# Kernel optimization log

Hardware: AMD Instinct MI355X
Metric: run time of the kernel (lower is better)

Reference implementation:

```python
import jax, jax.numpy as jnp
import numpy as np

B, L, D, H = 4, 1024, 1024, 16
DH = D // H
NEG = -1e9
EPS = 1e-5


def setup_inputs() -> dict:
    key = jax.random.key(0)
    ks = jax.random.split(key, 12)
    s = 1.0 / np.sqrt(D)
    inp = {
        "Q": jax.random.normal(ks[0], (B, L, D), jnp.float32),
        "K": jax.random.normal(ks[1], (B, L, D), jnp.float32),
        "V": jax.random.normal(ks[2], (B, L, D), jnp.float32),
        "K_mask": jnp.ones((B, L), jnp.int32),
        "WQ": jax.random.normal(ks[3], (D, D), jnp.float32) * s,
        "bQ": jnp.zeros((D,), jnp.float32),
        "WK": jax.random.normal(ks[4], (D, D), jnp.float32) * s,
        "bK": jnp.zeros((D,), jnp.float32),
        "WV": jax.random.normal(ks[5], (D, D), jnp.float32) * s,
        "bV": jnp.zeros((D,), jnp.float32),
        "WO": jax.random.normal(ks[6], (D, D), jnp.float32) * s,
        "bO": jnp.zeros((D,), jnp.float32),
        "ln_g": jnp.ones((D,), jnp.float32),
        "ln_b": jnp.zeros((D,), jnp.float32),
    }
    return inp


def _mha(Q, K, V, K_mask, WQ, bQ, WK, bK, WV, bV, WO, bO, ln_g, ln_b):
    # projections  [B,L,D]
    q = Q @ WQ + bQ
    k = K @ WK + bK
    v = V @ WV + bV
    # split heads -> [B,H,L,dh]
    q = q.reshape(B, L, H, DH).transpose(0, 2, 1, 3)
    k = k.reshape(B, L, H, DH).transpose(0, 2, 1, 3)
    v = v.reshape(B, L, H, DH).transpose(0, 2, 1, 3)
    # scaled dot product, masked softmax over keys
    scores = jnp.einsum("bhqd,bhkd->bhqk", q, k) / jnp.sqrt(jnp.float32(DH))
    mask = (K_mask > 0)[:, None, None, :]  # [B,1,1,Lk]
    scores = jnp.where(mask, scores, NEG)
    attn = jax.nn.softmax(scores, axis=-1)  # dropout is identity at inference
    ctx = jnp.einsum("bhqk,bhkd->bhqd", attn, v)
    ctx = ctx.transpose(0, 2, 1, 3).reshape(B, L, D)
    # output layer: dense + residual + layernorm
    out = ctx @ WO + bO
    x = out + Q
    mu = jnp.mean(x, axis=-1, keepdims=True)
    var = jnp.var(x, axis=-1, keepdims=True)
    return (x - mu) * jax.lax.rsqrt(var + EPS) * ln_g + ln_b


def reference(Q, K, V, K_mask, WQ, bQ, WK, bK, WV, bV, WO, bO, ln_g, ln_b):
    return _mha(Q, K, V, K_mask, WQ, bQ, WK, bK, WV, bV, WO, bO, ln_g, ln_b)
```

## Files before the change

### kernel.cpp

```cpp
#include <hip/hip_runtime.h>
#include <hip/hip_bf16.h>
#include <stdint.h>

#define Bn 4
#define Ln 1024
#define Dn 1024
#define Hn 16
#define DHn 64
#define Mn (Bn*Ln)

typedef __attribute__((ext_vector_type(8))) short short8v;
typedef __attribute__((ext_vector_type(4))) float floatx4;

__device__ __forceinline__ unsigned short f2b(float f){
  union { float f; unsigned u; } v; v.f = f;
  unsigned r = (v.u + 0x7FFFu + ((v.u >> 16) & 1u)) >> 16;
  return (unsigned short)r;
}
__device__ __forceinline__ unsigned short f2b_fast(float f){
  __hip_bfloat16 h = __float2bfloat16(f);
  return *reinterpret_cast<unsigned short*>(&h);
}

typedef const unsigned __attribute__((address_space(1)))* gas1_t;
typedef unsigned __attribute__((address_space(3)))* las3_t;
__device__ __forceinline__ void gload16(const void* g, void* l){
  __builtin_amdgcn_global_load_lds((gas1_t)(uintptr_t)g, (las3_t)(uintptr_t)l, 16, 0, 0);
}

__global__ __launch_bounds__(256) void tobf16x3_k(const float* __restrict__ x0,
    const float* __restrict__ x1, const float* __restrict__ x2,
    unsigned short* __restrict__ o0, unsigned short* __restrict__ o1,
    unsigned short* __restrict__ o2)
{
  const int i = blockIdx.x * 256 + threadIdx.x;
  const int sel = i >> 20, idx = i & 0xFFFFF;
  const float* x = sel == 0 ? x0 : (sel == 1 ? x1 : x2);
  unsigned short* o = sel == 0 ? o0 : (sel == 1 ? o1 : o2);
  float4 v = reinterpret_cast<const float4*>(x)[idx];
  union { unsigned short u[4]; uint2 q; } p;
  p.u[0] = f2b(v.x); p.u[1] = f2b(v.y); p.u[2] = f2b(v.z); p.u[3] = f2b(v.w);
  reinterpret_cast<uint2*>(o)[idx] = p.q;
}

__global__ __launch_bounds__(256) void wconv4_k(const float* __restrict__ W0,
    const float* __restrict__ W1, const float* __restrict__ W2,
    const float* __restrict__ W3, unsigned short* __restrict__ Wt0,
    unsigned short* __restrict__ Wt1, unsigned short* __restrict__ Wt2,
    unsigned short* __restrict__ Wt3)
{
  const float* W; unsigned short* Wt;
  switch (blockIdx.z){
    case 0: W = W0; Wt = Wt0; break;
    case 1: W = W1; Wt = Wt1; break;
    case 2: W = W2; Wt = Wt2; break;
    default: W = W3; Wt = Wt3; break;
  }
  __shared__ float tile[64][65];
  const int nb = blockIdx.x * 64, kb = blockIdx.y * 64;
  const int tx = threadIdx.x & 63, ty = threadIdx.x >> 6;
  #pragma unroll
  for (int r = 0; r < 64; r += 4)
    tile[r + ty][tx] = W[(size_t)(kb + r + ty) * 1024 + nb + tx];
  __syncthreads();
  #pragma unroll
  for (int r = 0; r < 64; r += 4)
    Wt[(size_t)(nb + r + ty) * 1024 + kb + tx] = f2b(tile[tx][r + ty]);
}

template<int MODE>
__device__ __forceinline__ void gemm8_core(const unsigned short* __restrict__ Ab,
    const unsigned short* __restrict__ Btp, const float* __restrict__ bias,
    void* __restrict__ outp, float scale, unsigned short* lds, int nt, int mt)
{
  const int tid = threadIdx.x;
  const int lane = tid & 63, wave = tid >> 6;
  const int wr = wave >> 2, wc = wave & 3;
  const int lg = lane >> 4, lr = lane & 15;
  const int m0 = mt * 256, n0 = nt * 256;

  const unsigned short* gAb[2];
  const unsigned short* gBb[2];
  int ldso[2];
  #pragma unroll
  for (int i = 0; i < 2; i++){
    int c = tid + 512 * i;
    int g16 = c >> 6, lrr = c & 15, lgg = (c >> 4) & 3;
    int row = g16 * 16 + lrr;
    gAb[i] = Ab  + (size_t)(m0 + row) * 1024 + lgg * 8;
    gBb[i] = Btp + (size_t)(n0 + row) * 1024 + lgg * 8;
    ldso[i] = c * 8;
  }
  auto stageA = [&](int sg){
    unsigned short* slot = lds + (sg & 3) * 16384;
    const int kcol = (sg >> 1) * 64 + (sg & 1) * 32;
    #pragma unroll
    for (int i = 0; i < 2; i++) gload16(gAb[i] + kcol, &slot[ldso[i]]);
  };
  auto stageB = [&](int sg){
    unsigned short* slot = lds + (sg & 3) * 16384 + 8192;
    const int kcol = (sg >> 1) * 64 + (sg & 1) * 32;
    #pragma unroll
    for (int i = 0; i < 2; i++) gload16(gBb[i] + kcol, &slot[ldso[i]]);
  };

  floatx4 acc[8][4] = {};

  stageA(0); stageB(0); stageA(1); stageB(1); stageA(2); stageB(2);

  for (int t = 0; t < 16; t++){
    unsigned short* slot0 = lds + ((2 * t) & 3) * 16384;
    unsigned short* slot1 = lds + ((2 * t + 1) & 3) * 16384;
    short8v af[4], bf[4];
    if (t < 15) asm volatile("s_waitcnt vmcnt(4)" ::: "memory");
    else        asm volatile("s_waitcnt vmcnt(0)" ::: "memory");
    __builtin_amdgcn_s_barrier();
    __builtin_amdgcn_sched_barrier(0);
    if (t < 15) stageA(2 * t + 3);
    #pragma unroll
    for (int n = 0; n < 4; n++)
      bf[n] = *reinterpret_cast<const short8v*>(&slot0[8192 + ((wc * 4 + n) * 64 + lane) * 8]);
    #pragma unroll
    for (int i2 = 0; i2 < 4; i2++)
      af[i2] = *reinterpret_cast<const short8v*>(&slot0[((wr * 8 + i2) * 64 + lane) * 8]);
    __builtin_amdgcn_s_setprio(1);
    #pragma unroll
    for (int a = 0; a < 4; a++)
      #pragma unroll
      for (int n = 0; n < 4; n++)
        acc[a][n] = __builtin_amdgcn_mfma_f32_16x16x32_bf16(af[a], bf[n], acc[a][n], 0, 0, 0);
    __builtin_amdgcn_s_setprio(0);
    if (t < 15) stageB(2 * t + 3);
    #pragma unroll
    for (int i2 = 0; i2 < 4; i2++)
      af[i2] = *reinterpret_cast<const short8v*>(&slot0[((wr * 8 + 4 + i2) * 64 + lane) * 8]);
    __builtin_amdgcn_s_setprio(1);
    #pragma unroll
    for (int a = 0; a < 4; a++)
      #pragma unroll
      for (int n = 0; n < 4; n++)
        acc[4 + a][n] = __builtin_amdgcn_mfma_f32_16x16x32_bf16(af[a], bf[n], acc[4 + a][n], 0, 0, 0);
    __builtin_amdgcn_s_setprio(0);
    __builtin_amdgcn_sched_barrier(0);
    __builtin_amdgcn_s_barrier();
    __builtin_amdgcn_sched_barrier(0);
    if (t < 14) stageA(2 * t + 4);
    #pragma unroll
    for (int n = 0; n < 4; n++)
      bf[n] = *reinterpret_cast<const short8v*>(&slot1[8192 + ((wc * 4 + n) * 64 + lane) * 8]);
    #pragma unroll
    for (int i2 = 0; i2 < 4; i2++)
      af[i2] = *reinterpret_cast<const short8v*>(&slot1[((wr * 8 + i2) * 64 + lane) * 8]);
    __builtin_amdgcn_s_setprio(1);
    #pragma unroll
    for (int a = 0; a < 4; a++)
      #pragma unroll
      for (int n = 0; n < 4; n++)
        acc[a][n] = __builtin_amdgcn_mfma_f32_16x16x32_bf16(af[a], bf[n], acc[a][n], 0, 0, 0);
    __builtin_amdgcn_s_setprio(0);
    if (t < 14) stageB(2 * t + 4);
    #pragma unroll
    for (int i2 = 0; i2 < 4; i2++)
      af[i2] = *reinterpret_cast<const short8v*>(&slot1[((wr * 8 + 4 + i2) * 64 + lane) * 8]);
    __builtin_amdgcn_s_setprio(1);
    #pragma unroll
    for (int a = 0; a < 4; a++)
      #pragma unroll
      for (int n = 0; n < 4; n++)
        acc[4 + a][n] = __builtin_amdgcn_mfma_f32_16x16x32_bf16(af[a], bf[n], acc[4 + a][n], 0, 0, 0);
    __builtin_amdgcn_s_setprio(0);
    __builtin_amdgcn_sched_barrier(0);
  }

  if constexpr (MODE == 2){
    __syncthreads();
    #pragma unroll
    for (int n = 0; n < 4; n++){
      const int gn_l = wc * 64 + n * 16 + lr;
      const float bb = bias[n0 + gn_l];
      const int X = (gn_l & 7) << 3;
      #pragma unroll
      for (int a = 0; a < 8; a++){
        const int gm_l = wr * 128 + a * 16 + lg * 4;
        union { unsigned short u[4]; uint2 q; } pk;
        #pragma unroll
        for (int r = 0; r < 4; r++) pk.u[r] = f2b((acc[a][n][r] + bb) * scale);
        *reinterpret_cast<uint2*>(&lds[gn_l * 256 + (gm_l ^ X)]) = pk.q;
      }
    }
    __syncthreads();
    const int bb2 = m0 >> 10, l0 = m0 & 1023;
    const int row = tid >> 1, colb = (tid & 1) * 128;
    const int h2 = (n0 + row) >> 6, d = (n0 + row) & 63;
    unsigned short* obase = (unsigned short*)outp +
        (((size_t)(bb2 * Hn + h2)) * DHn + d) * Ln + l0 + colb;
    const int XR = (row & 7) << 3;
    #pragma unroll
    for (int g = 0; g < 16; g++){
      short8v v = *reinterpret_cast<const short8v*>(&lds[row * 256 + ((colb + g * 8) ^ XR)]);
      *reinterpret_cast<short8v*>(obase + g * 8) = v;
    }
  } else {
    unsigned short* o = (unsigned short*)outp;
    #pragma unroll
    for (int n = 0; n < 4; n++){
      const int gn = n0 + wc * 64 + n * 16 + lr;
      const float bbv = bias[gn];
      const int h2 = gn >> 6, d = gn & 63;
      #pragma unroll
      for (int a = 0; a < 8; a++){
        const int gm0v = m0 + wr * 128 + a * 16 + lg * 4;
        #pragma unroll
        for (int r = 0; r < 4; r++){
          const int gm = gm0v + r;
          const int bb2 = gm >> 10, l = gm & 1023;
          o[(((size_t)(bb2 * Hn + h2)) * Ln + l) * DHn + d] = f2b((acc[a][n][r] + bbv) * scale);
        }
      }
    }
  }
}

__global__ __launch_bounds__(512, 2) void gemmqkv8_k(
    const unsigned short* __restrict__ A0, const unsigned short* __restrict__ A1,
    const unsigned short* __restrict__ A2, const unsigned short* __restrict__ W0,
    const unsigned short* __restrict__ W1, const unsigned short* __restrict__ W2,
    const float* __restrict__ b0, const float* __restrict__ b1,
    const float* __restrict__ b2, unsigned short* __restrict__ o0,
    unsigned short* __restrict__ o1, unsigned short* __restrict__ o2, float qscl)
{
  __shared__ __align__(16) unsigned short lds[65536];
  const int g = blockIdx.x >> 3;
  const int nt = g & 3;
  const int panel = (g >> 2) * 8 + (blockIdx.x & 7);
  const int z = panel >> 4, mt = panel & 15;
  if (z == 0)
    gemm8_core<0>(A0, W0, b0, o0, qscl, lds, nt, mt);
  else if (z == 1)
    gemm8_core<0>(A1, W1, b1, o1, 1.f, lds, nt, mt);
  else
    gemm8_core<2>(A2, W2, b2, o2, 1.f, lds, nt, mt);
}

__device__ __forceinline__ void gemm_core3(const unsigned short* __restrict__ Ab,
    const unsigned short* __restrict__ Btp, const float* __restrict__ bias,
    float* __restrict__ outp, const float* __restrict__ resid,
    unsigned short* lds, int nt, int mt)
{
  const int tid = threadIdx.x;
  const int lane = tid & 63, wave = tid >> 6;
  const int wr = wave >> 1, wc = wave & 1;
  const int lg = lane >> 4, lr = lane & 15;
  const int m0 = mt * 128, n0 = nt * 128;

  const unsigned short* gA[4];
  const unsigned short* gB[4];
  #pragma unroll
  for (int i = 0; i < 4; i++){
    int c = (wave * 4 + i) * 64 + lane;
    int ks = c >> 9, r16 = (c >> 6) & 7, lhi = (c >> 4) & 3, lrr = c & 15;
    int row = r16 * 16 + lrr, col = ks * 32 + lhi * 8;
    gA[i] = Ab  + (size_t)(m0 + row) * 1024 + col;
    gB[i] = Btp + (size_t)(n0 + row) * 1024 + col;
  }

  floatx4 acc[4][4] = {};

  auto issue = [&](int t){
    unsigned short* bufA = lds + (t % 3) * 16384;
    unsigned short* bufB = bufA + 8192;
    #pragma unroll
    for (int i = 0; i < 4; i++){
      gload16(gA[i] + t * 64, &bufA[(wave * 4 + i) * 512]);
      gload16(gB[i] + t * 64, &bufB[(wave * 4 + i) * 512]);
    }
  };

  issue(0); issue(1);

  for (int kb = 0; kb < 16; kb++){
    unsigned short* bufA = lds + (kb % 3) * 16384;
    unsigned short* bufB = bufA + 8192;
    if (kb < 14){
      issue(kb + 2);
      asm volatile("s_waitcnt vmcnt(16)" ::: "memory");
    } else if (kb == 14){
      asm volatile("s_waitcnt vmcnt(8)" ::: "memory");
    } else {
      asm volatile("s_waitcnt vmcnt(0)" ::: "memory");
    }
    __builtin_amdgcn_s_barrier();
    __builtin_amdgcn_sched_barrier(0);
    #pragma unroll
    for (int ks = 0; ks < 2; ks++){
      short8v af[4], bfr[4];
      #pragma unroll
      for (int m = 0; m < 4; m++)
        af[m] = *reinterpret_cast<const short8v*>(&bufA[((ks * 8 + wr * 4 + m) * 64 + lane) * 8]);
      #pragma unroll
      for (int n = 0; n < 4; n++)
        bfr[n] = *reinterpret_cast<const short8v*>(&bufB[((ks * 8 + wc * 4 + n) * 64 + lane) * 8]);
      #pragma unroll
      for (int m = 0; m < 4; m++)
        #pragma unroll
        for (int n = 0; n < 4; n++)
          acc[m][n] = __builtin_amdgcn_mfma_f32_16x16x32_bf16(af[m], bfr[n], acc[m][n], 0, 0, 0);
    }
    __builtin_amdgcn_sched_barrier(0);
    __builtin_amdgcn_s_barrier();
  }

  #pragma unroll
  for (int n = 0; n < 4; n++){
    const int gn = n0 + wc * 64 + n * 16 + lr;
    const float bb = bias[gn];
    #pragma unroll
    for (int m = 0; m < 4; m++){
      const int gm0 = m0 + wr * 64 + m * 16 + lg * 4;
      #pragma unroll
      for (int r = 0; r < 4; r++){
        const int gm = gm0 + r;
        float v = acc[m][n][r] + bb;
        outp[(size_t)gm * Dn + gn] = v + resid[(size_t)gm * Dn + gn];
      }
    }
  }
}

__global__ __launch_bounds__(256) void gemmo_k(const unsigned short* __restrict__ Ab,
    const unsigned short* __restrict__ W, const float* __restrict__ bias,
    float* __restrict__ out, const float* __restrict__ resid)
{
  __shared__ __align__(16) unsigned short lds[49152];
  const int bid = blockIdx.x;
  const int xcd = bid & 7, k = bid >> 3;
  const int mt = xcd * 4 + (k >> 3);
  const int nt = k & 7;
  gemm_core3(Ab, W, bias, out, resid, lds, nt, mt);
}

__global__ __launch_bounds__(256) void attn_k(const unsigned short* __restrict__ qb,
    const unsigned short* __restrict__ kbf, const unsigned short* __restrict__ vtb,
    const int* __restrict__ kmask, unsigned short* __restrict__ ctx)
{
  const int bh = blockIdx.x;
  const int qt = blockIdx.y;
  const int b = bh >> 4, h = bh & 15;
  const int tid = threadIdx.x;
  const int w = tid >> 6, lane = tid & 63;
  const int lg = lane >> 4, lr = lane & 15;

  const unsigned short* qp = qb  + (size_t)bh * Ln * DHn;
  const unsigned short* kp = kbf + (size_t)bh * Ln * DHn;
  const unsigned short* vp = vtb + (size_t)bh * DHn * Ln;
  const int q0 = qt * 128 + w * 32;

  __shared__ __align__(16) unsigned short ldsK[2][4096];
  __shared__ __align__(16) unsigned short ldsV[2][4096];
  __shared__ __align__(16) unsigned short plds[4][32][72];

  const unsigned short* gK[2];
  const unsigned short* gV[2];
  #pragma unroll
  for (int i = 0; i < 2; i++){
    int bc = w * 2 + i;
    int ks = bc >> 2, j = bc & 3;
    int row = j * 16 + lr, col = ks * 32 + lg * 8;
    gK[i] = kp + (size_t)row * DHn + col;
    gV[i] = vp + (size_t)row * Ln  + col;
  }

  short8v aq[2][2];
  #pragma unroll
  for (int f = 0; f < 2; f++)
    #pragma unroll
    for (int ks = 0; ks < 2; ks++)
      aq[f][ks] = *reinterpret_cast<const short8v*>(
          qp + (size_t)(q0 + f * 16 + lr) * DHn + ks * 32 + lg * 8);

  floatx4 accO[2][4] = {};
  float lsacc[2][4] = {{0.f,0.f,0.f,0.f},{0.f,0.f,0.f,0.f}};

  const int* mrow = kmask + b * Ln;
  int mkA[4], mkB[4];

  #pragma unroll
  for (int i = 0; i < 2; i++){
    gload16(gK[i], &ldsK[0][(w * 2 + i) * 512]);
    gload16(gV[i], &ldsV[0][(w * 2 + i) * 512]);
  }
  #pragma unroll
  for (int j = 0; j < 4; j++) mkA[j] = mrow[j * 16 + lr];

  for (int t = 0; t < 16; t++){
    const int cur = t & 1;
    asm volatile("s_waitcnt vmcnt(0)" ::: "memory");
    __syncthreads();
    if (t < 15){
      #pragma unroll
      for (int i = 0; i < 2; i++){
        gload16(gK[i] + (size_t)(t + 1) * 4096, &ldsK[cur ^ 1][(w * 2 + i) * 512]);
        gload16(gV[i] + (size_t)(t + 1) * 64,   &ldsV[cur ^ 1][(w * 2 + i) * 512]);
      }
      #pragma unroll
      for (int j = 0; j < 4; j++) mkB[j] = mrow[(t + 1) * 64 + j * 16 + lr];
    }

    floatx4 s[2][4] = {};
    #pragma unroll
    for (int ks = 0; ks < 2; ks++)
      #pragma unroll
      for (int j = 0; j < 4; j++){
        short8v bk = *reinterpret_cast<const short8v*>(&ldsK[cur][((ks * 4 + j) * 64 + lane) * 8]);
        s[0][j] = __builtin_amdgcn_mfma_f32_16x16x32_bf16(aq[0][ks], bk, s[0][j], 0, 0, 0);
        s[1][j] = __builtin_amdgcn_mfma_f32_16x16x32_bf16(aq[1][ks], bk, s[1][j], 0, 0, 0);
      }
    if (__all(mkA[0] > 0 && mkA[1] > 0 && mkA[2] > 0 && mkA[3] > 0)){
      #pragma unroll
      for (int f = 0; f < 2; f++)
        #pragma unroll
        for (int j = 0; j < 4; j++)
          #pragma unroll
          for (int r = 0; r < 4; r++){
            float p = __builtin_amdgcn_exp2f(s[f][j][r]);
            lsacc[f][r] += p;
            plds[w][f * 16 + lg * 4 + r][j * 16 + lr] = f2b_fast(p);
          }
    } else {
      #pragma unroll
      for (int j = 0; j < 4; j++){
        const float madd = mkA[j] > 0 ? 0.f : -1e9f;
        #pragma unroll
        for (int f = 0; f < 2; f++)
          #pragma unroll
          for (int r = 0; r < 4; r++){
            float p = __builtin_amdgcn_exp2f(s[f][j][r] + madd);
            lsacc[f][r] += p;
            plds[w][f * 16 + lg * 4 + r][j * 16 + lr] = f2b_fast(p);
          }
      }
    }
    #pragma unroll
    for (int ks = 0; ks < 2; ks++){
      short8v pa0 = *reinterpret_cast<const short8v*>(&plds[w][lr][ks * 32 + lg * 8]);
      short8v pa1 = *reinterpret_cast<const short8v*>(&plds[w][16 + lr][ks * 32 + lg * 8]);
      #pragma unroll
      for (int n = 0; n < 4; n++){
        short8v bv = *reinterpret_cast<const short8v*>(&ldsV[cur][((ks * 4 + n) * 64 + lane) * 8]);
        accO[0][n] = __builtin_amdgcn_mfma_f32_16x16x32_bf16(pa0, bv, accO[0][n], 0, 0, 0);
        accO[1][n] = __builtin_amdgcn_mfma_f32_16x16x32_bf16(pa1, bv, accO[1][n], 0, 0, 0);
      }
    }
    #pragma unroll
    for (int j = 0; j < 4; j++) mkA[j] = mkB[j];
  }

  #pragma unroll
  for (int f = 0; f < 2; f++)
    #pragma unroll
    for (int r = 0; r < 4; r++){
      lsacc[f][r] += __shfl_xor(lsacc[f][r], 1, 64);
      lsacc[f][r] += __shfl_xor(lsacc[f][r], 2, 64);
      lsacc[f][r] += __shfl_xor(lsacc[f][r], 4, 64);
      lsacc[f][r] += __shfl_xor(lsacc[f][r], 8, 64);
      lsacc[f][r] = 1.f / fmaxf(lsacc[f][r], 1e-20f);
    }
  #pragma unroll
  for (int f = 0; f < 2; f++)
    #pragma unroll
    for (int n = 0; n < 4; n++)
      #pragma unroll
      for (int r = 0; r < 4; r++){
        float o = accO[f][n][r] * lsacc[f][r];
        int q = q0 + f * 16 + lg * 4 + r;
        ctx[((size_t)(b * Ln + q)) * Dn + h * DHn + n * 16 + lr] = f2b_fast(o);
      }
}

__global__ __launch_bounds__(256) void ln_k(const float* __restrict__ x,
    const float* __restrict__ g, const float* __restrict__ bt, float* __restrict__ out)
{
  const int row = blockIdx.x;
  const int tid = threadIdx.x;
  float4 v = *reinterpret_cast<const float4*>(x + (size_t)row * 1024 + tid * 4);
  float s  = v.x + v.y + v.z + v.w;
  float sq = v.x * v.x + v.y * v.y + v.z * v.z + v.w * v.w;
  #pragma unroll
  for (int off = 32; off >= 1; off >>= 1){
    s  += __shfl_xor(s, off, 64);
    sq += __shfl_xor(sq, off, 64);
  }
  __shared__ float psm[4], pqm[4];
  const int w = tid >> 6;
  if ((tid & 63) == 0){ psm[w] = s; pqm[w] = sq; }
  __syncthreads();
  s  = psm[0] + psm[1] + psm[2] + psm[3];
  sq = pqm[0] + pqm[1] + pqm[2] + pqm[3];
  const float mean = s * (1.f / 1024.f);
  const float var  = sq * (1.f / 1024.f) - mean * mean;
  const float inv  = rsqrtf(var + 1e-5f);
  float4 gg = *reinterpret_cast<const float4*>(g  + tid * 4);
  float4 bb = *reinterpret_cast<const float4*>(bt + tid * 4);
  float4 o;
  o.x = (v.x - mean) * inv * gg.x + bb.x;
  o.y = (v.y - mean) * inv * gg.y + bb.y;
  o.z = (v.z - mean) * inv * gg.z + bb.z;
  o.w = (v.w - mean) * inv * gg.w + bb.w;
  *reinterpret_cast<float4*>(out + (size_t)row * 1024 + tid * 4) = o;
}

extern "C" void kernel_launch(void* const* d_in, const int* in_sizes, int n_in,
                              void* d_out, int out_size, void* d_ws, size_t ws_size,
                              hipStream_t stream)
{
  const float* Qin = (const float*)d_in[0];
  const float* Kin = (const float*)d_in[1];
  const float* Vin = (const float*)d_in[2];
  const int*   Kms = (const int*)d_in[3];
  const float* WQ  = (const float*)d_in[4];
  const float* bQ  = (const float*)d_in[5];
  const float* WK  = (const float*)d_in[6];
  const float* bK  = (const float*)d_in[7];
  const float* WV  = (const float*)d_in[8];
  const float* bV  = (const float*)d_in[9];
  const float* WO  = (const float*)d_in[10];
  const float* bO  = (const float*)d_in[11];
  const float* lng = (const float*)d_in[12];
  const float* lnb = (const float*)d_in[13];

  char* ws = (char*)d_ws;
  const size_t MB = 1024u * 1024u;
  unsigned short* wqt = (unsigned short*)(ws + 0 * MB);
  unsigned short* wkt = (unsigned short*)(ws + 2 * MB);
  unsigned short* wvt = (unsigned short*)(ws + 4 * MB);
  unsigned short* wot = (unsigned short*)(ws + 6 * MB);
  unsigned short* qbf = (unsigned short*)(ws + 8 * MB);
  unsigned short* kbf = (unsigned short*)(ws + 16 * MB);
  unsigned short* vtb = (unsigned short*)(ws + 24 * MB);
  unsigned short* ctx = (unsigned short*)(ws + 32 * MB);
  float*          xbf = (float*)(ws + 40 * MB);
  unsigned short* cv0 = (unsigned short*)(ws + 32 * MB);
  unsigned short* cv1 = (unsigned short*)(ws + 40 * MB);
  unsigned short* cv2 = (unsigned short*)(ws + 48 * MB);

  dim3 blk(256);
  wconv4_k<<<dim3(16, 16, 4), blk, 0, stream>>>(WQ, WK, WV, WO, wqt, wkt, wvt, wot);
  tobf16x3_k<<<12288, blk, 0, stream>>>(Qin, Kin, Vin, cv0, cv1, cv2);

  const float QSCL = 0.125f * 1.44269504088896f;
  gemmqkv8_k<<<192, dim3(512), 0, stream>>>(cv0, cv1, cv2, wqt, wkt, wvt,
                                            bQ, bK, bV, qbf, kbf, vtb, QSCL);

  attn_k<<<dim3(64, 8), blk, 0, stream>>>(qbf, kbf, vtb, Kms, ctx);

  gemmo_k<<<256, blk, 0, stream>>>(ctx, wot, bO, xbf, Qin);

  ln_k<<<4096, blk, 0, stream>>>(xbf, lng, lnb, (float*)d_out);
}
```

Baseline: 120.3 us.

## Rework output-projection GEMM pipeline into 4-stage ring with single barrier

The output projection GEMM now streams K in 32-wide stages through a 4-slot LDS ring (previously 64-wide stages in 3 slots), keeping three stages in flight. It drops the trailing barrier per iteration by issuing the next load after the leading barrier, and raises wave priority around the MFMA block. The aim is to cut barrier overhead and LDS footprint to improve latency hiding or occupancy, at the cost of twice as many loop iterations with less MFMA work between syncs.

After: 120.4 us. About the same (+0.1%).

```diff
diff --git a/kernel.cpp b/kernel.cpp
--- a/kernel.cpp
+++ b/kernel.cpp
@@ -242,72 +242,70 @@
     gemm8_core<2>(A2, W2, b2, o2, 1.f, lds, nt, mt);
 }
 
-__device__ __forceinline__ void gemm_core3(const unsigned short* __restrict__ Ab,
-    const unsigned short* __restrict__ Btp, const float* __restrict__ bias,
-    float* __restrict__ outp, const float* __restrict__ resid,
-    unsigned short* lds, int nt, int mt)
-{
+__global__ __launch_bounds__(256) void gemmo_k(const unsigned short* __restrict__ Ab,
+    const unsigned short* __restrict__ W, const float* __restrict__ bias,
+    float* __restrict__ out, const float* __restrict__ resid)
+{
+  __shared__ __align__(16) unsigned short lds[32768];
+  const int bid = blockIdx.x;
+  const int xcd = bid & 7, k = bid >> 3;
+  const int mt = xcd * 4 + (k >> 3);
+  const int nt = k & 7;
+
   const int tid = threadIdx.x;
   const int lane = tid & 63, wave = tid >> 6;
   const int wr = wave >> 1, wc = wave & 1;
   const int lg = lane >> 4, lr = lane & 15;
   const int m0 = mt * 128, n0 = nt * 128;
 
-  const unsigned short* gA[4];
-  const unsigned short* gB[4];
-  #pragma unroll
-  for (int i = 0; i < 4; i++){
-    int c = (wave * 4 + i) * 64 + lane;
-    int ks = c >> 9, r16 = (c >> 6) & 7, lhi = (c >> 4) & 3, lrr = c & 15;
-    int row = r16 * 16 + lrr, col = ks * 32 + lhi * 8;
-    gA[i] = Ab  + (size_t)(m0 + row) * 1024 + col;
-    gB[i] = Btp + (size_t)(n0 + row) * 1024 + col;
-  }
+  const unsigned short* gA[2];
+  const unsigned short* gB[2];
+  int ldso[2];
+  #pragma unroll
+  for (int i = 0; i < 2; i++){
+    int c = tid + 256 * i;
+    int g16 = c >> 6, lrr = c & 15, lgg = (c >> 4) & 3;
+    int row = g16 * 16 + lrr;
+    gA[i] = Ab + (size_t)(m0 + row) * 1024 + lgg * 8;
+    gB[i] = W  + (size_t)(n0 + row) * 1024 + lgg * 8;
+    ldso[i] = c * 8;
+  }
+  auto issue = [&](int s){
+    unsigned short* base = lds + (s & 3) * 8192;
+    const int kc = s * 32;
+    #pragma unroll
+    for (int i = 0; i < 2; i++) gload16(gA[i] + kc, &base[ldso[i]]);
+    #pragma unroll
+    for (int i = 0; i < 2; i++) gload16(gB[i] + kc, &base[4096 + ldso[i]]);
+  };
 
   floatx4 acc[4][4] = {};
 
-  auto issue = [&](int t){
-    unsigned short* bufA = lds + (t % 3) * 16384;
-    unsigned short* bufB = bufA + 8192;
-    #pragma unroll
-    for (int i = 0; i < 4; i++){
-      gload16(gA[i] + t * 64, &bufA[(wave * 4 + i) * 512]);
-      gload16(gB[i] + t * 64, &bufB[(wave * 4 + i) * 512]);
-    }
-  };
-
-  issue(0); issue(1);
-
-  for (int kb = 0; kb < 16; kb++){
-    unsigned short* bufA = lds + (kb % 3) * 16384;
-    unsigned short* bufB = bufA + 8192;
-    if (kb < 14){
-      issue(kb + 2);
-      asm volatile("s_waitcnt vmcnt(16)" ::: "memory");
-    } else if (kb == 14){
-      asm volatile("s_waitcnt vmcnt(8)" ::: "memory");
-    } else {
-      asm volatile("s_waitcnt vmcnt(0)" ::: "memory");
-    }
+  issue(0); issue(1); issue(2);
+
+  for (int s = 0; s < 32; s++){
+    unsigned short* base = lds + (s & 3) * 8192;
+    if (s <= 29)      asm volatile("s_waitcnt vmcnt(8)" ::: "memory");
+    else if (s == 30) asm volatile("s_waitcnt vmcnt(4)" ::: "memory");
+    else              asm volatile("s_waitcnt vmcnt(0)" ::: "memory");
     __builtin_amdgcn_s_barrier();
     __builtin_amdgcn_sched_barrier(0);
-    #pragma unroll
-    for (int ks = 0; ks < 2; ks++){
-      short8v af[4], bfr[4];
-      #pragma unroll
-      for (int m = 0; m < 4; m++)
-        af[m] = *reinterpret_cast<const short8v*>(&bufA[((ks * 8 + wr * 4 + m) * 64 + lane) * 8]);
+    if (s <= 28) issue(s + 3);
+    short8v af[4], bf[4];
+    #pragma unroll
+    for (int m = 0; m < 4; m++)
+      af[m] = *reinterpret_cast<const short8v*>(&base[((wr * 4 + m) * 64 + lane) * 8]);
+    #pragma unroll
+    for (int n = 0; n < 4; n++)
+      bf[n] = *reinterpret_cast<const short8v*>(&base[4096 + ((wc * 4 + n) * 64 + lane) * 8]);
+    __builtin_amdgcn_s_setprio(1);
+    #pragma unroll
+    for (int m = 0; m < 4; m++)
       #pragma unroll
       for (int n = 0; n < 4; n++)
-        bfr[n] = *reinterpret_cast<const short8v*>(&bufB[((ks * 8 + wc * 4 + n) * 64 + lane) * 8]);
-      #pragma unroll
-      for (int m = 0; m < 4; m++)
-        #pragma unroll
-        for (int n = 0; n < 4; n++)
-          acc[m][n] = __builtin_amdgcn_mfma_f32_16x16x32_bf16(af[m], bfr[n], acc[m][n], 0, 0, 0);
-    }
+        acc[m][n] = __builtin_amdgcn_mfma_f32_16x16x32_bf16(af[m], bf[n], acc[m][n], 0, 0, 0);
+    __builtin_amdgcn_s_setprio(0);
     __builtin_amdgcn_sched_barrier(0);
-    __builtin_amdgcn_s_barrier();
   }
 
   #pragma unroll
@@ -320,23 +318,10 @@
       #pragma unroll
       for (int r = 0; r < 4; r++){
         const int gm = gm0 + r;
-        float v = acc[m][n][r] + bb;
-        outp[(size_t)gm * Dn + gn] = v + resid[(size_t)gm * Dn + gn];
-      }
-    }
-  }
-}
-
-__global__ __launch_bounds__(256) void gemmo_k(const unsigned short* __restrict__ Ab,
-    const unsigned short* __restrict__ W, const float* __restrict__ bias,
-    float* __restrict__ out, const float* __restrict__ resid)
-{
-  __shared__ __align__(16) unsigned short lds[49152];
-  const int bid = blockIdx.x;
-  const int xcd = bid & 7, k = bid >> 3;
-  const int mt = xcd * 4 + (k >> 3);
-  const int nt = k & 7;
-  gemm_core3(Ab, W, bias, out, resid, lds, nt, mt);
+        out[(size_t)gm * Dn + gn] = acc[m][n][r] + bb + resid[(size_t)gm * Dn + gn];
+      }
+    }
+  }
 }
 
 __global__ __launch_bounds__(256) void attn_k(const unsigned short* __restrict__ qb,
```
